# Kernel optimization log

Hardware: AMD Instinct MI355X
Metric: run time of the kernel (lower is better)

The kernel has to match this reference:

```python
import jax, jax.numpy as jnp
import numpy as np

H = 256      # hidden_dim
MEL = 80     # num_mel
R = 5        # reduction_factor
BS = 128
T_ENC = 512
T_DEC = 1000


def _gru_step(x, h, wih, whh, bih, bhh):
    # PyTorch GRU cell: gates order (r, z, n)
    gi = x @ wih.T + bih            # [bs, 3H]
    gh = h @ whh.T + bhh
    ir, iz, inn = jnp.split(gi, 3, axis=-1)
    hr, hz, hn = jnp.split(gh, 3, axis=-1)
    r = jax.nn.sigmoid(ir + hr)
    z = jax.nn.sigmoid(iz + hz)
    n = jnp.tanh(inn + r * hn)
    return (1.0 - z) * n + z * h


def setup_inputs() -> dict:
    key = jax.random.key(0)
    ks = iter(jax.random.split(key, 40))
    s = 0.05
    def w(shape):
        return jax.random.normal(next(ks), shape, dtype=jnp.float32) * s
    inp = {
        "enc_vec": jax.random.normal(next(ks), (BS, T_ENC, H), dtype=jnp.float32),
        "decoder_input": jax.random.normal(next(ks), (BS, T_DEC, MEL), dtype=jnp.float32),
        # Pre_net
        "pre_w1": w((H, MEL)), "pre_b1": jnp.zeros((H,), jnp.float32),
        "pre_w2": w((H // 2, H)), "pre_b2": jnp.zeros((H // 2,), jnp.float32),
        # Bahdanau attention
        "w1": w((H, H)), "b1": jnp.zeros((H,), jnp.float32),
        "w2": w((H, H)), "b2": jnp.zeros((H,), jnp.float32),
        "v_w": w((1, H)), "v_b": jnp.zeros((1,), jnp.float32),
        # projection and output
        "proj_w": w((H, 2 * H)), "proj_b": jnp.zeros((H,), jnp.float32),
        "out_w": w((MEL * R, H)), "out_b": jnp.zeros((MEL * R,), jnp.float32),
        # Attention GRU (input H//2)
        "att_wih": w((3 * H, H // 2)), "att_whh": w((3 * H, H)),
        "att_bih": jnp.zeros((3 * H,), jnp.float32), "att_bhh": jnp.zeros((3 * H,), jnp.float32),
        # GRU1, GRU2 (input H)
        "g1_wih": w((3 * H, H)), "g1_whh": w((3 * H, H)),
        "g1_bih": jnp.zeros((3 * H,), jnp.float32), "g1_bhh": jnp.zeros((3 * H,), jnp.float32),
        "g2_wih": w((3 * H, H)), "g2_whh": w((3 * H, H)),
        "g2_bih": jnp.zeros((3 * H,), jnp.float32), "g2_bhh": jnp.zeros((3 * H,), jnp.float32),
    }
    return inp


def reference(enc_vec, decoder_input, pre_w1, pre_b1, pre_w2, pre_b2,
              w1, b1, w2, b2, v_w, v_b, proj_w, proj_b, out_w, out_b,
              att_wih, att_whh, att_bih, att_bhh,
              g1_wih, g1_whh, g1_bih, g1_bhh,
              g2_wih, g2_whh, g2_bih, g2_bhh):
    bs = enc_vec.shape[0]
    # Pre_net (dropout omitted -> deterministic eval behavior)
    pre = jax.nn.relu(decoder_input @ pre_w1.T + pre_b1)
    pre = jax.nn.relu(pre @ pre_w2.T + pre_b2)          # [bs, T_dec, H//2]
    steps = decoder_input.shape[1] // R                 # 200
    # teacher-forced inputs: step i uses pre[:, i*R, :]
    xs = jnp.transpose(pre[:, :steps * R:R, :], (1, 0, 2))   # [steps, bs, H//2]
    # hoist W1(enc_vec): constant across decoder steps
    w1enc = enc_vec @ w1.T + b1                         # [bs, T_enc, H]

    h0 = jnp.zeros((bs, H), jnp.float32)

    def step(carry, x):
        ha, h1, h2 = carry
        d = _gru_step(x, ha, att_wih, att_whh, att_bih, att_bhh)   # [bs, H]
        e = jnp.tanh(w1enc + (d @ w2.T + b2)[:, None, :])          # [bs, T_enc, H]
        scores = e @ v_w[0] + v_b[0]                               # [bs, T_enc]
        u = jax.nn.softmax(scores, axis=1)
        d_dot = jnp.einsum('bt,bth->bh', u, enc_vec)               # [bs, H]
        p = jnp.concatenate([d, d_dot], axis=-1) @ proj_w.T + proj_b  # [bs, H]
        o1 = _gru_step(p, h1, g1_wih, g1_whh, g1_bih, g1_bhh)
        in2 = o1 + p
        o2 = _gru_step(in2, h2, g2_wih, g2_whh, g2_bih, g2_bhh)
        out = (in2 + o2) @ out_w.T + out_b                         # [bs, R*MEL]
        return (d, o1, o2), out

    _, ys = jax.lax.scan(step, (h0, h0, h0), xs)        # [steps, bs, R*MEL]
    ys = jnp.transpose(ys, (1, 0, 2)).reshape(bs, steps * R, MEL)
    return ys
```

## Files before the change

kernel.cpp:

```cpp
#include <hip/hip_runtime.h>
#include <hip/hip_bf16.h>

typedef unsigned short u16;
typedef unsigned int   u32;

constexpr int H     = 256;
constexpr int HH    = 128;
constexpr int MELD  = 80;
constexpr int RF    = 5;
constexpr int BS    = 128;
constexpr int TENC  = 512;
constexpr int TDEC  = 1000;
constexpr int STEPS = 200;
constexpr int OD    = 400;
constexpr int M_ALL = STEPS * BS;

constexpr size_t GI_B   = 0;
constexpr size_t ENC16_B= GI_B;
constexpr size_t D16_B  = GI_B   + (size_t)M_ALL*768*4;
constexpr size_t IN2_B  = D16_B;
constexpr size_t W1ET_B = D16_B  + (size_t)M_ALL*512*2;
constexpr size_t P16_B  = W1ET_B;
constexpr size_t IN2H_B = W1ET_B + (size_t)M_ALL*256*2;
constexpr size_t P_B    = W1ET_B + (size_t)BS*H*TENC*2;
constexpr size_t U16_B  = P_B;
constexpr size_t XSH_B  = P_B    + (size_t)M_ALL*256*4;
constexpr size_t ST16_B = XSH_B  + (size_t)M_ALL*128*2;
constexpr size_t WPK_B  = ST16_B + (size_t)M_ALL*256*2;
constexpr size_t WH_B   = WPK_B  + 3*(size_t)393216;
constexpr size_t WH_AW  = 0;
constexpr size_t WH_W2  = WH_AW + 98304*2;
constexpr size_t WH_PJ  = WH_W2 + 65536*2;
constexpr size_t WH_G1  = WH_PJ + 131072*2;
constexpr size_t WH_G2  = WH_G1 + 196608*2;
constexpr size_t WH_OW  = WH_G2 + 196608*2;
constexpr size_t WH_W1  = WH_OW + 102400*2;
constexpr size_t WH_END = WH_W1 + 65536*2;
constexpr size_t NEED_FAST = WH_B + WH_END;

constexpr size_t FBW1E_B  = 65536;
constexpr size_t FBXST_B  = FBW1E_B + (size_t)BS*TENC*H*2;
constexpr size_t FBF32_B  = FBXST_B + (size_t)STEPS*HH*BS*2;
constexpr size_t FBDT_F   = 0;
constexpr size_t FBO1_F   = FBDT_F + 2*(size_t)H*BS;
constexpr size_t FBO2_F   = FBO1_F + 2*(size_t)H*BS;
constexpr size_t FBPT_F   = FBO2_F + 2*(size_t)H*BS;
constexpr size_t FBIN2_F  = FBPT_F + (size_t)H*BS;
constexpr size_t FBST_F   = FBIN2_F + (size_t)H*BS;
constexpr size_t FB_NEED_B = FBF32_B + (FBST_F + 2*(size_t)H*BS) * 4;

__device__ __forceinline__ float bf2f(u16 v) {
  union { u32 x; float f; } c; c.x = ((u32)v) << 16; return c.f;
}
__device__ __forceinline__ float bfu_lo(u32 u) { union { u32 x; float f; } c; c.x = u << 16;        return c.f; }
__device__ __forceinline__ float bfu_hi(u32 u) { union { u32 x; float f; } c; c.x = u & 0xffff0000u; return c.f; }
__device__ __forceinline__ u16 f2bf(float f) {
  union { float f; u32 u; } c; c.f = f;
  u32 u = c.u;
  u32 r = (u + 0x7fffu + ((u >> 16) & 1u)) >> 16;
  return (u16)r;
}
__device__ __forceinline__ u16 f2h(float f) {
  union { _Float16 h; u16 u; } c; c.h = (_Float16)f; return c.u;
}
__device__ __forceinline__ float fexp(float x) {
  return __builtin_amdgcn_exp2f(1.4426950408889634f * x);
}
__device__ __forceinline__ float sigm_f(float x) {
  return __builtin_amdgcn_rcpf(1.0f + __builtin_amdgcn_exp2f(-1.4426950408889634f * x));
}
__device__ __forceinline__ float tanh_f(float x) {
  x = fminf(fmaxf(x, -15.f), 15.f);
  float e = __builtin_amdgcn_exp2f(2.8853900817779268f * x);
  return (e - 1.0f) * __builtin_amdgcn_rcpf(e + 1.0f);
}

typedef _Float16 hlf2 __attribute__((ext_vector_type(2)));
typedef _Float16 f16x8 __attribute__((ext_vector_type(8)));
typedef float f32x4 __attribute__((ext_vector_type(4)));

__global__ __launch_bounds__(256) void k_zero(float* __restrict__ out, int n) {
  int i = blockIdx.x * 256 + threadIdx.x;
  if (i < n) out[i] = 0.f;
}


__global__ __launch_bounds__(256) void k_prenet_f(
    const float* __restrict__ dec, const float* __restrict__ w1, const float* __restrict__ b1,
    const float* __restrict__ w2, const float* __restrict__ b2, u16* __restrict__ xsh)
{
  const int s = blockIdx.x, tid = threadIdx.x;
  __shared__ float X0[32][80];
  __shared__ float P1t[32][256];
  for (int bt = 0; bt < 4; ++bt) {
    const int b0 = bt * 32;
    __syncthreads();
    for (int i = tid; i < 32 * 80; i += 256) {
      int bb = i / 80, m = i - bb * 80;
      X0[bb][m] = dec[((size_t)(b0 + bb) * TDEC + (size_t)s * RF) * MELD + m];
    }
    __syncthreads();
    {
      const int h = tid;
      float acc[32];
      const float bias = b1[h];
      #pragma unroll
      for (int r = 0; r < 32; ++r) acc[r] = bias;
      const float* wr = w1 + (size_t)h * MELD;
      for (int m = 0; m < 80; m += 4) {
        float4 wv = *(const float4*)(wr + m);
        #pragma unroll
        for (int r = 0; r < 32; ++r) {
          float4 x = *(const float4*)&X0[r][m];
          acc[r] += x.x * wv.x + x.y * wv.y + x.z * wv.z + x.w * wv.w;
        }
      }
      #pragma unroll
      for (int r = 0; r < 32; ++r) P1t[r][h] = fmaxf(acc[r], 0.f);
    }
    __syncthreads();
    {
      const int k = tid & 127, bh = tid >> 7;
      float acc[16];
      const float bias = b2[k];
      #pragma unroll
      for (int r = 0; r < 16; ++r) acc[r] = bias;
      const float* wr = w2 + (size_t)k * H;
      for (int h = 0; h < H; h += 4) {
        float4 wv = *(const float4*)(wr + h);
        #pragma unroll
        for (int r = 0; r < 16; ++r) {
          float4 x = *(const float4*)&P1t[bh * 16 + r][h];
          acc[r] += x.x * wv.x + x.y * wv.y + x.z * wv.z + x.w * wv.w;
        }
      }
      #pragma unroll
      for (int r = 0; r < 16; ++r)
        xsh[((size_t)s * BS + b0 + bh * 16 + r) * HH + k] = f2h(fmaxf(acc[r], 0.f));
    }
  }
}

__global__ __launch_bounds__(256) void k_packall(
    const float* __restrict__ enc, u16* __restrict__ enc16,
    const float* __restrict__ awhh, const float* __restrict__ g1whh,
    const float* __restrict__ g2whh, u32* __restrict__ wpk,
    const float* __restrict__ awih, u16* __restrict__ awih16,
    const float* __restrict__ w2w,  u16* __restrict__ w2w16,
    const float* __restrict__ pjw,  u16* __restrict__ pjw16,
    const float* __restrict__ g1wih, u16* __restrict__ g1w16,
    const float* __restrict__ g2wih, u16* __restrict__ g2w16,
    const float* __restrict__ ow,   u16* __restrict__ ow16,
    const float* __restrict__ w1w,  u16* __restrict__ w1w16)
{
  int i = blockIdx.x * 256 + threadIdx.x;
  if (i < 16777216) { enc16[i] = f2h(enc[i]); return; }
  i -= 16777216;
  if (i < 294912) {
    int which = i / 98304, idx = i - which * 98304;
    const float* w = which == 0 ? awhh : (which == 1 ? g1whh : g2whh);
    int q  = idx & 3;
    int l  = (idx >> 2) & 63;
    int kt = (idx >> 8) & 7;
    int nt = idx >> 11;
    int col = nt * 16 + (l & 15);
    int k   = kt * 32 + (l >> 4) * 8 + 2 * q;
    union { _Float16 f[2]; u32 u; } c;
    c.f[0] = (_Float16)w[(size_t)col * 256 + k];
    c.f[1] = (_Float16)w[(size_t)col * 256 + k + 1];
    wpk[which * 98304 + idx] = c.u;
    return;
  }
  i -= 294912;
  if (i < 98304)  { awih16[i] = f2h(awih[i]); return; }  i -= 98304;
  if (i < 65536)  { w2w16[i]  = f2h(w2w[i]);  return; }  i -= 65536;
  if (i < 131072) { pjw16[i]  = f2h(pjw[i]);  return; }  i -= 131072;
  if (i < 196608) { g1w16[i]  = f2h(g1wih[i]); return; } i -= 196608;
  if (i < 196608) { g2w16[i]  = f2h(g2wih[i]); return; } i -= 196608;
  if (i < 102400) { ow16[i]   = f2h(ow[i]);   return; }  i -= 102400;
  if (i < 65536)  { w1w16[i]  = f2h(w1w[i]);  return; }
}
constexpr int PACKALL_N = 16777216 + 294912 + 856064;

__global__ __launch_bounds__(256) void k_hgemm(
    const u16* __restrict__ A, int lda,
    const u16* __restrict__ W, int K,
    const float* __restrict__ bias,
    float* __restrict__ C, u16* __restrict__ Ch, int ldc, int N,
    float* __restrict__ outmap, u16* __restrict__ CbfT)
{
  __shared__ _Float16 As[128 * 40];
  __shared__ _Float16 Ws[64 * 40];
  const int m0 = blockIdx.y * 128, n0 = blockIdx.x * 64;
  const int tid = threadIdx.x;
  const int wv = tid >> 6, lane = tid & 63;
  const int l15 = lane & 15, hi = lane >> 4;
  f32x4 acc[2][4];
  #pragma unroll
  for (int mi = 0; mi < 2; ++mi)
    #pragma unroll
    for (int ni = 0; ni < 4; ++ni) acc[mi][ni] = (f32x4){0.f, 0.f, 0.f, 0.f};

  const int ar = tid >> 1, ac = (tid & 1) * 16;
  const int wr = tid >> 2, wc = (tid & 3) * 8;
  for (int k0 = 0; k0 < K; k0 += 32) {
    __syncthreads();
    {
      const u16* src = A + (size_t)(m0 + ar) * lda + k0 + ac;
      uint4 v0 = *(const uint4*)(src);
      uint4 v1 = *(const uint4*)(src + 8);
      *(uint4*)&As[ar * 40 + ac] = v0;
      *(uint4*)&As[ar * 40 + ac + 8] = v1;
    }
    {
      uint4 v;
      if (n0 + wr < N) v = *(const uint4*)(W + (size_t)(n0 + wr) * K + k0 + wc);
      else { v.x = v.y = v.z = v.w = 0u; }
      *(uint4*)&Ws[wr * 40 + wc] = v;
    }
    __syncthreads();
    f16x8 af[2], bf[4];
    #pragma unroll
    for (int mi = 0; mi < 2; ++mi)
      af[mi] = *(const f16x8*)&As[(wv * 32 + mi * 16 + l15) * 40 + hi * 8];
    #pragma unroll
    for (int ni = 0; ni < 4; ++ni)
      bf[ni] = *(const f16x8*)&Ws[(ni * 16 + l15) * 40 + hi * 8];
    #pragma unroll
    for (int mi = 0; mi < 2; ++mi)
      #pragma unroll
      for (int ni = 0; ni < 4; ++ni)
        acc[mi][ni] = __builtin_amdgcn_mfma_f32_16x16x32_f16(af[mi], bf[ni], acc[mi][ni], 0, 0, 0);
  }
  const int gm = m0 + wv * 32;
  #pragma unroll
  for (int ni = 0; ni < 4; ++ni) {
    const int col = n0 + ni * 16 + l15;
    if (col < N) {
      const float bv = bias[col];
      #pragma unroll
      for (int mi = 0; mi < 2; ++mi) {
        #pragma unroll
        for (int r = 0; r < 4; ++r) {
          const int row = gm + mi * 16 + hi * 4 + r;
          float v = acc[mi][ni][r] + bv;
          if (outmap) {
            int s = row >> 7, b = row & 127;
            int fr = s * RF + col / MELD, mel = col - (col / MELD) * MELD;
            outmap[((size_t)b * TDEC + fr) * MELD + mel] = v;
          } else if (CbfT) {
            float a = fminf(fmaxf(2.8853900817779268f * v, -15.f), 15.f);
            CbfT[(((size_t)(row >> 9) * 256 + col) << 9) + (row & 511)] =
                f2bf(__builtin_amdgcn_exp2f(a));
          } else {
            if (C)  C[(size_t)row * ldc + col] = v;
            if (Ch) Ch[(size_t)row * ldc + col] = f2h(v);
          }
        }
      }
    }
  }
}

__global__ __launch_bounds__(256) void k_ddgemm(
    const u16* __restrict__ U, const float* __restrict__ enc,
    u16* __restrict__ D16)
{
  __shared__ _Float16 As[128 * 40];
  __shared__ _Float16 Ws[64 * 40];
  const int b = blockIdx.z;
  const int m0 = blockIdx.y * 128, n0 = blockIdx.x * 64;
  const int tid = threadIdx.x;
  const int wv = tid >> 6, lane = tid & 63;
  const int l15 = lane & 15, hi = lane >> 4;
  f32x4 acc[2][4];
  #pragma unroll
  for (int mi = 0; mi < 2; ++mi)
    #pragma unroll
    for (int ni = 0; ni < 4; ++ni) acc[mi][ni] = (f32x4){0.f, 0.f, 0.f, 0.f};

  const u16* A = U + (size_t)b * STEPS * TENC;
  const float* E = enc + (size_t)b * TENC * H;
  const int ar = tid >> 1, ac = (tid & 1) * 16;
  for (int k0 = 0; k0 < TENC; k0 += 32) {
    __syncthreads();
    {
      const u16* src = A + (size_t)(m0 + ar) * TENC + k0 + ac;
      uint4 v0 = *(const uint4*)(src);
      uint4 v1 = *(const uint4*)(src + 8);
      *(uint4*)&As[ar * 40 + ac] = v0;
      *(uint4*)&As[ar * 40 + ac + 8] = v1;
    }
    {
      #pragma unroll
      for (int it = 0; it < 2; ++it) {
        int flat = tid + it * 256;
        int kk = flat >> 4, hc4 = (flat & 15) * 4;
        float4 v = *(const float4*)(E + (size_t)(k0 + kk) * H + n0 + hc4);
        Ws[(hc4 + 0) * 40 + kk] = (_Float16)v.x;
        Ws[(hc4 + 1) * 40 + kk] = (_Float16)v.y;
        Ws[(hc4 + 2) * 40 + kk] = (_Float16)v.z;
        Ws[(hc4 + 3) * 40 + kk] = (_Float16)v.w;
      }
    }
    __syncthreads();
    f16x8 af[2], bf[4];
    #pragma unroll
    for (int mi = 0; mi < 2; ++mi)
      af[mi] = *(const f16x8*)&As[(wv * 32 + mi * 16 + l15) * 40 + hi * 8];
    #pragma unroll
    for (int ni = 0; ni < 4; ++ni)
      bf[ni] = *(const f16x8*)&Ws[(ni * 16 + l15) * 40 + hi * 8];
    #pragma unroll
    for (int mi = 0; mi < 2; ++mi)
      #pragma unroll
      for (int ni = 0; ni < 4; ++ni)
        acc[mi][ni] = __builtin_amdgcn_mfma_f32_16x16x32_f16(af[mi], bf[ni], acc[mi][ni], 0, 0, 0);
  }
  const int gm = m0 + wv * 32;
  #pragma unroll
  for (int ni = 0; ni < 4; ++ni) {
    const int col = n0 + ni * 16 + l15;
    #pragma unroll
    for (int mi = 0; mi < 2; ++mi) {
      #pragma unroll
      for (int r = 0; r < 4; ++r) {
        const int row = gm + mi * 16 + hi * 4 + r;
        if (row < STEPS)
          D16[((size_t)(row * BS + b)) * 512 + 256 + col] = f2h(acc[mi][ni][r]);
      }
    }
  }
}

__global__ __launch_bounds__(512) void k_chain(
    const float* __restrict__ gi,
    const uint4* __restrict__ wpkB,
    const float* __restrict__ bhh,
    const float* __restrict__ addsrc,
    int astride,
    float* __restrict__ outp, int ostride,
    u16* __restrict__ outph, int ostrideh)
{
  const int b = blockIdx.x, tid = threadIdx.x;
  const int wv = tid >> 6, lane = tid & 63;
  const int l15 = lane & 15, hi = lane >> 4;
  __shared__ __align__(16) _Float16 hf[256];
  __shared__ float gsh[768];
  f16x8 bfrag[6][8];
  #pragma unroll
  for (int nti = 0; nti < 6; ++nti)
    #pragma unroll
    for (int kt = 0; kt < 8; ++kt)
      bfrag[nti][kt] = *(const f16x8*)&wpkB[(((size_t)(wv * 6 + nti) * 8 + kt) * 64 + lane)];
  if (tid < 256) hf[tid] = (_Float16)0.f;
  const int j = tid;
  float br = 0.f, bz = 0.f, bn = 0.f, hreg = 0.f;
  float gr = 0.f, gz = 0.f, gn = 0.f, av = 0.f;
  if (tid < 256) {
    br = bhh[j]; bz = bhh[256 + j]; bn = bhh[512 + j];
    const float* gim = gi + (size_t)b * 768;
    gr = gim[j]; gz = gim[256 + j]; gn = gim[512 + j];
    if (addsrc) av = addsrc[(size_t)b * astride + j];
  }
  __syncthreads();
  for (int s = 0; s < STEPS; ++s) {
    f32x4 acc[6];
    #pragma unroll
    for (int nti = 0; nti < 6; ++nti) acc[nti] = (f32x4){0.f, 0.f, 0.f, 0.f};
    #pragma unroll
    for (int kt = 0; kt < 8; ++kt) {
      f16x8 af = *(const f16x8*)&hf[kt * 32 + hi * 8];
      #pragma unroll
      for (int nti = 0; nti < 6; ++nti)
        acc[nti] = __builtin_amdgcn_mfma_f32_16x16x32_f16(af, bfrag[nti][kt], acc[nti], 0, 0, 0);
    }
    float gr_n = 0.f, gz_n = 0.f, gn_n = 0.f, av_n = 0.f;
    if (tid < 256 && s + 1 < STEPS) {
      const size_t mn = (size_t)(s + 1) * BS + b;
      const float* gim = gi + mn * 768;
      gr_n = gim[j]; gz_n = gim[256 + j]; gn_n = gim[512 + j];
      if (addsrc) av_n = addsrc[mn * astride + j];
    }
    if (hi == 0) {
      #pragma unroll
      for (int nti = 0; nti < 6; ++nti)
        gsh[(wv * 6 + nti) * 16 + l15] = acc[nti][0];
    }
    __syncthreads();
    if (tid < 256) {
      const size_t m = (size_t)s * BS + b;
      float ar = gsh[j], az = gsh[256 + j], an = gsh[512 + j];
      float r = sigm_f(gr + ar + br);
      float z = sigm_f(gz + az + bz);
      float n = tanh_f(gn + r * (an + bn));
      float hn_ = (1.f - z) * n + z * hreg;
      hreg = hn_;
      hf[j] = (_Float16)hn_;
      float ov = hn_ + av;
      if (outp)  outp[m * ostride + j] = ov;
      if (outph) outph[m * ostrideh + j] = f2h(ov);
    }
    __syncthreads();
    gr = gr_n; gz = gz_n; gn = gn_n; av = av_n;
  }
}

constexpr int ATT_ST = 10;
__global__ __launch_bounds__(256) void k_att(
    const u16* __restrict__ w1eT, const float* __restrict__ Q,
    const float* __restrict__ vw_, u16* __restrict__ U16)
{
  const int b = blockIdx.x, s0 = blockIdx.y * ATT_ST, tid = threadIdx.x;
  __shared__ float qt[ATT_ST][260];
  __shared__ float vws[256];
  __shared__ float redw[ATT_ST][4];
  vws[tid] = -2.0f * vw_[tid];
  #pragma unroll
  for (int si = 0; si < ATT_ST; ++si) {
    float q = 2.8853900817779268f * Q[((size_t)(s0 + si) * BS + b) * H + tid];
    qt[si][tid] = __builtin_amdgcn_exp2f(fminf(fmaxf(q, -15.f), 15.f));
  }
  __syncthreads();

  float sc0[ATT_ST], sc1[ATT_ST];
  #pragma unroll
  for (int si = 0; si < ATT_ST; ++si) { sc0[si] = 0.f; sc1[si] = 0.f; }
  const u32* wrow = (const u32*)w1eT + (size_t)b * H * (TENC / 2);
  for (int h = 0; h < H; h += 4) {
    u32 wa = wrow[(size_t)(h + 0) * 256 + tid];
    u32 wb = wrow[(size_t)(h + 1) * 256 + tid];
    u32 wc = wrow[(size_t)(h + 2) * 256 + tid];
    u32 wd = wrow[(size_t)(h + 3) * 256 + tid];
    float Ea0 = bfu_lo(wa), Ea1 = bfu_hi(wa);
    float Eb0 = bfu_lo(wb), Eb1 = bfu_hi(wb);
    float Ec0 = bfu_lo(wc), Ec1 = bfu_hi(wc);
    float Ed0 = bfu_lo(wd), Ed1 = bfu_hi(wd);
    float4 vv = *(const float4*)&vws[h];
    #pragma unroll
    for (int si = 0; si < ATT_ST; ++si) {
      float4 Eq = *(const float4*)&qt[si][h];
      {
        float F1 = __builtin_fmaf(Ea0, Eq.x, 1.f);
        float F2 = __builtin_fmaf(Eb0, Eq.y, 1.f);
        float F3 = __builtin_fmaf(Ec0, Eq.z, 1.f);
        float F4 = __builtin_fmaf(Ed0, Eq.w, 1.f);
        float P12 = F1 * F2, P34 = F3 * F4;
        float u12 = __builtin_fmaf(vv.y, F1, vv.x * F2);
        float u34 = __builtin_fmaf(vv.w, F3, vv.z * F4);
        float num = __builtin_fmaf(P12, u34, P34 * u12);
        sc0[si] = __builtin_fmaf(num, __builtin_amdgcn_rcpf(P12 * P34), sc0[si]);
      }
      {
        float F1 = __builtin_fmaf(Ea1, Eq.x, 1.f);
        float F2 = __builtin_fmaf(Eb1, Eq.y, 1.f);
        float F3 = __builtin_fmaf(Ec1, Eq.z, 1.f);
        float F4 = __builtin_fmaf(Ed1, Eq.w, 1.f);
        float P12 = F1 * F2, P34 = F3 * F4;
        float u12 = __builtin_fmaf(vv.y, F1, vv.x * F2);
        float u34 = __builtin_fmaf(vv.w, F3, vv.z * F4);
        float num = __builtin_fmaf(P12, u34, P34 * u12);
        sc1[si] = __builtin_fmaf(num, __builtin_amdgcn_rcpf(P12 * P34), sc1[si]);
      }
    }
  }
  const int lane = tid & 63, wvi = tid >> 6;
  #pragma unroll
  for (int si = 0; si < ATT_ST; ++si) {
    float mw = fmaxf(sc0[si], sc1[si]);
    for (int off = 1; off < 64; off <<= 1) mw = fmaxf(mw, __shfl_xor(mw, off));
    if (lane == 0) redw[si][wvi] = mw;
  }
  __syncthreads();
  #pragma unroll
  for (int si = 0; si < ATT_ST; ++si) {
    float mx = fmaxf(fmaxf(redw[si][0], redw[si][1]), fmaxf(redw[si][2], redw[si][3]));
    sc0[si] = fexp(sc0[si] - mx);
    sc1[si] = fexp(sc1[si] - mx);
  }
  __syncthreads();
  #pragma unroll
  for (int si = 0; si < ATT_ST; ++si) {
    float sm = sc0[si] + sc1[si];
    for (int off = 1; off < 64; off <<= 1) sm += __shfl_xor(sm, off);
    if (lane == 0) redw[si][wvi] = sm;
  }
  __syncthreads();
  #pragma unroll
  for (int si = 0; si < ATT_ST; ++si) {
    float tot = redw[si][0] + redw[si][1] + redw[si][2] + redw[si][3];
    float li = __builtin_amdgcn_rcpf(tot);
    u32 pk = (u32)f2h(sc0[si] * li) | ((u32)f2h(sc1[si] * li) << 16);
    *(u32*)&U16[((size_t)b * STEPS + s0 + si) * TENC + 2 * tid] = pk;
  }
}

__global__ __launch_bounds__(256) void fbk_zeroinit(float* __restrict__ fst) {
  int i = blockIdx.x * 256 + threadIdx.x;
  if (i < H * BS)              fst[FBDT_F + i] = 0.f;
  else if (i < 2 * H * BS)     fst[FBO1_F + (i - H * BS)] = 0.f;
  else if (i < 3 * H * BS)     fst[FBO2_F + (i - 2 * H * BS)] = 0.f;
}

__global__ __launch_bounds__(256) void fbk_prenet(
    const float* __restrict__ dec, const float* __restrict__ w1, const float* __restrict__ b1,
    const float* __restrict__ w2, const float* __restrict__ b2, u16* __restrict__ xsT)
{
  const int s = blockIdx.x, tid = threadIdx.x;
  __shared__ float X0[32][80];
  __shared__ float P1t[32][256];
  for (int bt = 0; bt < 4; ++bt) {
    const int b0 = bt * 32;
    __syncthreads();
    for (int i = tid; i < 32 * 80; i += 256) {
      int bb = i / 80, m = i - bb * 80;
      X0[bb][m] = dec[((size_t)(b0 + bb) * TDEC + (size_t)s * RF) * MELD + m];
    }
    __syncthreads();
    {
      const int h = tid;
      float acc[32];
      const float bias = b1[h];
      #pragma unroll
      for (int r = 0; r < 32; ++r) acc[r] = bias;
      const float* wr = w1 + (size_t)h * MELD;
      for (int m = 0; m < 80; m += 4) {
        float4 wv = *(const float4*)(wr + m);
        #pragma unroll
        for (int r = 0; r < 32; ++r) {
          float4 x = *(const float4*)&X0[r][m];
          acc[r] += x.x * wv.x + x.y * wv.y + x.z * wv.z + x.w * wv.w;
        }
      }
      #pragma unroll
      for (int r = 0; r < 32; ++r) P1t[r][h] = fmaxf(acc[r], 0.f);
    }
    __syncthreads();
    {
      const int k = tid & 127, bh = tid >> 7;
      float acc[16];
      const float bias = b2[k];
      #pragma unroll
      for (int r = 0; r < 16; ++r) acc[r] = bias;
      const float* wr = w2 + (size_t)k * H;
      for (int h = 0; h < H; h += 4) {
        float4 wv = *(const float4*)(wr + h);
        #pragma unroll
        for (int r = 0; r < 16; ++r) {
          float4 x = *(const float4*)&P1t[bh * 16 + r][h];
          acc[r] += x.x * wv.x + x.y * wv.y + x.z * wv.z + x.w * wv.w;
        }
      }
      #pragma unroll
      for (int r = 0; r < 16; ++r)
        xsT[((size_t)s * HH + k) * BS + b0 + bh * 16 + r] = f2bf(fmaxf(acc[r], 0.f));
    }
  }
}

__global__ __launch_bounds__(256) void fbk_w1enc(
    const float* __restrict__ enc, const float* __restrict__ w1, const float* __restrict__ b1,
    u16* __restrict__ w1e)
{
  const int row0 = blockIdx.x * 32;
  const int tid = threadIdx.x;
  __shared__ float A[32 * 256];
  for (int i = tid * 4; i < 32 * 256; i += 256 * 4) {
    float4 v = *(const float4*)(enc + (size_t)row0 * H + i);
    A[i] = v.x; A[i + 1] = v.y; A[i + 2] = v.z; A[i + 3] = v.w;
  }
  __syncthreads();
  const int h = tid;
  float acc[32];
  const float bias = b1[h];
  #pragma unroll
  for (int r = 0; r < 32; ++r) acc[r] = bias;
  const float* wr = w1 + (size_t)h * H;
  for (int k = 0; k < H; k += 4) {
    float4 wv = *(const float4*)(wr + k);
    #pragma unroll
    for (int r = 0; r < 32; ++r) {
      float4 a = *(const float4*)&A[r * 256 + k];
      acc[r] += a.x * wv.x + a.y * wv.y + a.z * wv.z + a.w * wv.w;
    }
  }
  #pragma unroll
  for (int r = 0; r < 32; ++r) w1e[((size_t)row0 + r) * H + h] = f2bf(acc[r]);
}

__device__ __forceinline__ void fb_gru_body(
    float (*w6)[260], float (*pA)[128], float (*pB)[128], int j, int tid,
    const float* __restrict__ gi_src, const float* __restrict__ h_src,
    const float* __restrict__ wih, const float* __restrict__ whh,
    const float* __restrict__ bih, const float* __restrict__ bhh,
    float* __restrict__ h_out, float* __restrict__ sum_out)
{
  for (int i = tid; i < 3 * H; i += 256) {
    int gg = i >> 8, k = i & 255;
    w6[gg][k]     = wih[((size_t)gg * H + j) * H + k];
    w6[3 + gg][k] = whh[((size_t)gg * H + j) * H + k];
  }
  __syncthreads();
  const int b = tid & 127, kh = tid >> 7;
  float pr = 0, pz = 0, pn = 0, hr = 0, hz = 0, hn = 0;
  for (int k = kh * 128; k < kh * 128 + 128; k += 4) {
    float4 wia = *(const float4*)&w6[0][k];
    float4 wib = *(const float4*)&w6[1][k];
    float4 wic = *(const float4*)&w6[2][k];
    float4 wha = *(const float4*)&w6[3][k];
    float4 whb = *(const float4*)&w6[4][k];
    float4 whc = *(const float4*)&w6[5][k];
    float x0 = gi_src[(size_t)(k + 0) * BS + b], x1 = gi_src[(size_t)(k + 1) * BS + b];
    float x2 = gi_src[(size_t)(k + 2) * BS + b], x3 = gi_src[(size_t)(k + 3) * BS + b];
    float h0 = h_src[(size_t)(k + 0) * BS + b],  h1 = h_src[(size_t)(k + 1) * BS + b];
    float h2 = h_src[(size_t)(k + 2) * BS + b],  h3 = h_src[(size_t)(k + 3) * BS + b];
    pr += x0 * wia.x + x1 * wia.y + x2 * wia.z + x3 * wia.w;
    pz += x0 * wib.x + x1 * wib.y + x2 * wib.z + x3 * wib.w;
    pn += x0 * wic.x + x1 * wic.y + x2 * wic.z + x3 * wic.w;
    hr += h0 * wha.x + h1 * wha.y + h2 * wha.z + h3 * wha.w;
    hz += h0 * whb.x + h1 * whb.y + h2 * whb.z + h3 * whb.w;
    hn += h0 * whc.x + h1 * whc.y + h2 * whc.z + h3 * whc.w;
  }
  if (kh) {
    pA[0][b] = pr; pA[1][b] = pz; pA[2][b] = pn;
    pB[0][b] = hr; pB[1][b] = hz; pB[2][b] = hn;
  }
  __syncthreads();
  if (!kh) {
    float gir = pr + pA[0][b] + bih[j];
    float giz = pz + pA[1][b] + bih[H + j];
    float gin = pn + pA[2][b] + bih[2 * H + j];
    float ghr = hr + pB[0][b] + bhh[j];
    float ghz = hz + pB[1][b] + bhh[H + j];
    float ghn = hn + pB[2][b] + bhh[2 * H + j];
    float r = sigm_f(gir + ghr);
    float z = sigm_f(giz + ghz);
    float n = tanh_f(gin + r * ghn);
    float hp = h_src[(size_t)j * BS + b];
    float o = (1.f - z) * n + z * hp;
    h_out[(size_t)j * BS + b] = o;
    if (sum_out) sum_out[(size_t)j * BS + b] = o + gi_src[(size_t)j * BS + b];
  }
}

__global__ __launch_bounds__(256) void fbk_attgru(
    const u16* __restrict__ xstu, float* __restrict__ fst,
    const float* __restrict__ awih, const float* __restrict__ awhh,
    const float* __restrict__ abih, const float* __restrict__ abhh, int s)
{
  const int j = blockIdx.x, tid = threadIdx.x;
  __shared__ float w6[6][260];
  __shared__ float pA[3][128];
  __shared__ float pB[3][128];
  const float* dprev = fst + FBDT_F + (size_t)(s & 1) * H * BS;
  float*       dcur  = fst + FBDT_F + (size_t)((s + 1) & 1) * H * BS;
  for (int i = tid; i < 3 * HH; i += 256) {
    int gg = i >> 7, k = i & (HH - 1);
    w6[gg][k] = awih[((size_t)gg * H + j) * HH + k];
  }
  for (int i = tid; i < 3 * H; i += 256) {
    int gg = i >> 8, k = i & (H - 1);
    w6[3 + gg][k] = awhh[((size_t)gg * H + j) * H + k];
  }
  __syncthreads();
  const u16* xcol = xstu + (size_t)s * HH * BS;
  const int b = tid & 127, kh = tid >> 7;
  float pr = 0, pz = 0, pn = 0, hr = 0, hz = 0, hn = 0;
  for (int k = kh * 64; k < kh * 64 + 64; k += 4) {
    float4 wa = *(const float4*)&w6[0][k];
    float4 wb = *(const float4*)&w6[1][k];
    float4 wc = *(const float4*)&w6[2][k];
    float x0 = bf2f(xcol[(size_t)(k + 0) * BS + b]), x1 = bf2f(xcol[(size_t)(k + 1) * BS + b]);
    float x2 = bf2f(xcol[(size_t)(k + 2) * BS + b]), x3 = bf2f(xcol[(size_t)(k + 3) * BS + b]);
    pr += x0 * wa.x + x1 * wa.y + x2 * wa.z + x3 * wa.w;
    pz += x0 * wb.x + x1 * wb.y + x2 * wb.z + x3 * wb.w;
    pn += x0 * wc.x + x1 * wc.y + x2 * wc.z + x3 * wc.w;
  }
  for (int k = kh * 128; k < kh * 128 + 128; k += 4) {
    float4 wa = *(const float4*)&w6[3][k];
    float4 wb = *(const float4*)&w6[4][k];
    float4 wc = *(const float4*)&w6[5][k];
    float h0 = dprev[(size_t)(k + 0) * BS + b], h1 = dprev[(size_t)(k + 1) * BS + b];
    float h2 = dprev[(size_t)(k + 2) * BS + b], h3 = dprev[(size_t)(k + 3) * BS + b];
    hr += h0 * wa.x + h1 * wa.y + h2 * wa.z + h3 * wa.w;
    hz += h0 * wb.x + h1 * wb.y + h2 * wb.z + h3 * wb.w;
    hn += h0 * wc.x + h1 * wc.y + h2 * wc.z + h3 * wc.w;
  }
  if (kh) {
    pA[0][b] = pr; pA[1][b] = pz; pA[2][b] = pn;
    pB[0][b] = hr; pB[1][b] = hz; pB[2][b] = hn;
  }
  __syncthreads();
  if (!kh) {
    float gir = pr + pA[0][b] + abih[j];
    float giz = pz + pA[1][b] + abih[H + j];
    float gin = pn + pA[2][b] + abih[2 * H + j];
    float ghr = hr + pB[0][b] + abhh[j];
    float ghz = hz + pB[1][b] + abhh[H + j];
    float ghn = hn + pB[2][b] + abhh[2 * H + j];
    float r = sigm_f(gir + ghr);
    float z = sigm_f(giz + ghz);
    float n = tanh_f(gin + r * ghn);
    float hp = dprev[(size_t)j * BS + b];
    dcur[(size_t)j * BS + b] = (1.f - z) * n + z * hp;
  }
}

__global__ __launch_bounds__(256) void fbk_attn(
    const float* __restrict__ enc, const u16* __restrict__ w1eu,
    const float* __restrict__ w2w, const float* __restrict__ b2w,
    const float* __restrict__ vww, const float* __restrict__ vbw,
    const float* __restrict__ pjw, const float* __restrict__ pjb,
    float* __restrict__ fst, int s)
{
  const int b3 = blockIdx.x, tid = threadIdx.x;
  __shared__ float dsh[256], qs[256], ddh[256], vwsh[256], ev[512], red[256];
  const float* dcur = fst + FBDT_F + (size_t)((s + 1) & 1) * H * BS;
  float* pT = fst + FBPT_F;
  dsh[tid]  = dcur[(size_t)tid * BS + b3];
  vwsh[tid] = vww[tid];
  __syncthreads();
  {
    const int jj = tid;
    const float* wr = w2w + (size_t)jj * H;
    float acc = b2w[jj];
    for (int k = 0; k < H; k += 8) {
      float4 wA = *(const float4*)(wr + k);
      float4 wB = *(const float4*)(wr + k + 4);
      float4 dA = *(const float4*)&dsh[k];
      float4 dB = *(const float4*)&dsh[k + 4];
      acc += dA.x * wA.x + dA.y * wA.y + dA.z * wA.z + dA.w * wA.w
           + dB.x * wB.x + dB.y * wB.y + dB.z * wB.z + dB.w * wB.w;
    }
    qs[jj] = acc;
  }
  __syncthreads();
  const float vbf = vbw[0];
  const u16* wr0 = w1eu + ((size_t)b3 * TENC + tid) * H;
  const u16* wr1 = wr0 + (size_t)256 * H;
  float sc0 = vbf, sc1 = vbf;
  for (int h = 0; h < H; h += 8) {
    uint4 ua = *(const uint4*)(wr0 + h);
    uint4 uc = *(const uint4*)(wr1 + h);
    float4 qA = *(const float4*)&qs[h];
    float4 qB = *(const float4*)&qs[h + 4];
    float4 vA = *(const float4*)&vwsh[h];
    float4 vB = *(const float4*)&vwsh[h + 4];
    sc0 += vA.x * tanh_f(bfu_lo(ua.x) + qA.x) + vA.y * tanh_f(bfu_hi(ua.x) + qA.y)
         + vA.z * tanh_f(bfu_lo(ua.y) + qA.z) + vA.w * tanh_f(bfu_hi(ua.y) + qA.w)
         + vB.x * tanh_f(bfu_lo(ua.z) + qB.x) + vB.y * tanh_f(bfu_hi(ua.z) + qB.y)
         + vB.z * tanh_f(bfu_lo(ua.w) + qB.z) + vB.w * tanh_f(bfu_hi(ua.w) + qB.w);
    sc1 += vA.x * tanh_f(bfu_lo(uc.x) + qA.x) + vA.y * tanh_f(bfu_hi(uc.x) + qA.y)
         + vA.z * tanh_f(bfu_lo(uc.y) + qA.z) + vA.w * tanh_f(bfu_hi(uc.y) + qA.w)
         + vB.x * tanh_f(bfu_lo(uc.z) + qB.x) + vB.y * tanh_f(bfu_hi(uc.z) + qB.y)
         + vB.z * tanh_f(bfu_lo(uc.w) + qB.z) + vB.w * tanh_f(bfu_hi(uc.w) + qB.w);
  }
  red[tid] = fmaxf(sc0, sc1);
  __syncthreads();
  for (int off = 128; off > 0; off >>= 1) {
    if (tid < off) red[tid] = fmaxf(red[tid], red[tid + off]);
    __syncthreads();
  }
  float mx = red[0];
  __syncthreads();
  float e0 = fexp(sc0 - mx), e1 = fexp(sc1 - mx);
  ev[tid] = e0; ev[256 + tid] = e1;
  red[tid] = e0 + e1;
  __syncthreads();
  for (int off = 128; off > 0; off >>= 1) {
    if (tid < off) red[tid] += red[tid + off];
    __syncthreads();
  }
  float linv = __builtin_amdgcn_rcpf(red[0]);
  __syncthreads();
  {
    float vacc = 0.f;
    const float* ep = enc + (size_t)b3 * TENC * H + tid;
    for (int tt = 0; tt < TENC; tt += 4) {
      float4 e4 = *(const float4*)&ev[tt];
      vacc += e4.x * ep[(size_t)(tt + 0) * H] + e4.y * ep[(size_t)(tt + 1) * H]
            + e4.z * ep[(size_t)(tt + 2) * H] + e4.w * ep[(size_t)(tt + 3) * H];
    }
    ddh[tid] = vacc * linv;
  }
  __syncthreads();
  {
    const int jj = tid;
    const float* wr = pjw + (size_t)jj * (2 * H);
    float acc = pjb[jj];
    for (int k = 0; k < H; k += 8) {
      float4 wA = *(const float4*)(wr + k);
      float4 wB = *(const float4*)(wr + k + 4);
      float4 dA = *(const float4*)&dsh[k];
      float4 dB = *(const float4*)&dsh[k + 4];
      acc += dA.x * wA.x + dA.y * wA.y + dA.z * wA.z + dA.w * wA.w
           + dB.x * wB.x + dB.y * wB.y + dB.z * wB.z + dB.w * wB.w;
    }
    for (int k = 0; k < H; k += 8) {
      float4 wA = *(const float4*)(wr + H + k);
      float4 wB = *(const float4*)(wr + H + k + 4);
      float4 dA = *(const float4*)&ddh[k];
      float4 dB = *(const float4*)&ddh[k + 4];
      acc += dA.x * wA.x + dA.y * wA.y + dA.z * wA.z + dA.w * wA.w
           + dB.x * wB.x + dB.y * wB.y + dB.z * wB.z + dB.w * wB.w;
    }
    pT[(size_t)jj * BS + b3] = acc;
  }
}

__global__ __launch_bounds__(256) void fbk_gru1(
    float* __restrict__ fst,
    const float* __restrict__ wih, const float* __restrict__ whh,
    const float* __restrict__ bih, const float* __restrict__ bhh, int s)
{
  __shared__ float w6[6][260];
  __shared__ float pA[3][128];
  __shared__ float pB[3][128];
  const float* pT     = fst + FBPT_F;
  const float* o1prev = fst + FBO1_F + (size_t)(s & 1) * H * BS;
  float*       o1cur  = fst + FBO1_F + (size_t)((s + 1) & 1) * H * BS;
  float*       in2T   = fst + FBIN2_F;
  fb_gru_body(w6, pA, pB, blockIdx.x, threadIdx.x, pT, o1prev, wih, whh, bih, bhh, o1cur, in2T);
}

__device__ __forceinline__ void fb_out_body(
    float (*pA)[128], int bb, int tid, int s,
    const float* __restrict__ sT, const float* __restrict__ ow,
    const float* __restrict__ ob, float* __restrict__ out)
{
  const int b = tid & 127, kh = tid >> 7;
  for (int r = bb; r < OD; r += 128) {
    const float* wr = ow + (size_t)r * H + kh * 128;
    float acc = 0.f;
    for (int kk = 0; kk < 128; kk += 4) {
      float4 wv = *(const float4*)(wr + kk);
      const float* sp = sT + (size_t)(kh * 128 + kk) * BS + b;
      acc += sp[0] * wv.x + sp[BS] * wv.y + sp[2 * BS] * wv.z + sp[3 * BS] * wv.w;
    }
    __syncthreads();
    if (kh) pA[0][b] = acc;
    __syncthreads();
    if (!kh) {
      float y = acc + pA[0][b] + ob[r];
      int frame = s * RF + r / MELD;
      int m = r - (r / MELD) * MELD;
      out[((size_t)b * TDEC + frame) * MELD + m] = y;
    }
  }
}

__global__ __launch_bounds__(256) void fbk_gru2out(
    float* __restrict__ fst,
    const float* __restrict__ wih, const float* __restrict__ whh,
    const float* __restrict__ bih, const float* __restrict__ bhh,
    const float* __restrict__ ow, const float* __restrict__ ob,
    float* __restrict__ out, int s)
{
  const int bid = blockIdx.x, tid = threadIdx.x;
  __shared__ float w6[6][260];
  __shared__ float pA[3][128];
  __shared__ float pB[3][128];
  if (bid < 256) {
    const float* in2T   = fst + FBIN2_F;
    const float* o2prev = fst + FBO2_F + (size_t)(s & 1) * H * BS;
    float*       o2cur  = fst + FBO2_F + (size_t)((s + 1) & 1) * H * BS;
    float*       stp    = fst + FBST_F + (size_t)(s & 1) * H * BS;
    fb_gru_body(w6, pA, pB, bid, tid, in2T, o2prev, wih, whh, bih, bhh, o2cur, stp);
  } else if (s > 0) {
    const float* sT = fst + FBST_F + (size_t)((s - 1) & 1) * H * BS;
    fb_out_body(pA, bid - 256, tid, s - 1, sT, ow, ob, out);
  }
}

__global__ __launch_bounds__(256) void fbk_outlast(
    const float* __restrict__ fst, const float* __restrict__ ow,
    const float* __restrict__ ob, float* __restrict__ out)
{
  __shared__ float pA[3][128];
  const float* sT = fst + FBST_F + (size_t)((STEPS - 1) & 1) * H * BS;
  fb_out_body(pA, blockIdx.x, threadIdx.x, STEPS - 1, sT, ow, ob, out);
}

extern "C" void kernel_launch(void* const* d_in, const int* in_sizes, int n_in,
                              void* d_out, int out_size, void* d_ws, size_t ws_size,
                              hipStream_t stream) {
  const float* enc   = (const float*)d_in[0];
  const float* dec   = (const float*)d_in[1];
  const float* pw1   = (const float*)d_in[2];
  const float* pb1   = (const float*)d_in[3];
  const float* pw2   = (const float*)d_in[4];
  const float* pb2   = (const float*)d_in[5];
  const float* w1w   = (const float*)d_in[6];
  const float* b1w   = (const float*)d_in[7];
  const float* w2w   = (const float*)d_in[8];
  const float* b2w   = (const float*)d_in[9];
  const float* vww   = (const float*)d_in[10];
  const float* vbw   = (const float*)d_in[11];
  const float* pjw   = (const float*)d_in[12];
  const float* pjb   = (const float*)d_in[13];
  const float* ow    = (const float*)d_in[14];
  const float* ob    = (const float*)d_in[15];
  const float* awih  = (const float*)d_in[16];
  const float* awhh  = (const float*)d_in[17];
  const float* abih  = (const float*)d_in[18];
  const float* abhh  = (const float*)d_in[19];
  const float* g1wih = (const float*)d_in[20];
  const float* g1whh = (const float*)d_in[21];
  const float* g1bih = (const float*)d_in[22];
  const float* g1bhh = (const float*)d_in[23];
  const float* g2wih = (const float*)d_in[24];
  const float* g2whh = (const float*)d_in[25];
  const float* g2bih = (const float*)d_in[26];
  const float* g2bhh = (const float*)d_in[27];
  float* out = (float*)d_out;
  char* wsb = (char*)d_ws;

  if (ws_size >= NEED_FAST) {
    float* GI   = (float*)(wsb + GI_B);
    u16*   ENC16= (u16*)(wsb + ENC16_B);
    u16*   D16  = (u16*)(wsb + D16_B);
    float* IN2  = (float*)(wsb + IN2_B);
    u16*   w1eT = (u16*)(wsb + W1ET_B);
    u16*   P16  = (u16*)(wsb + P16_B);
    u16*   IN2H = (u16*)(wsb + IN2H_B);
    float* P    = (float*)(wsb + P_B);
    u16*   U16  = (u16*)(wsb + U16_B);
    u16*   XSH  = (u16*)(wsb + XSH_B);
    u16*   ST16 = (u16*)(wsb + ST16_B);
    u32*   wpkA = (u32*)(wsb + WPK_B);
    u32*   wpk1 = wpkA + 98304;
    u32*   wpk2 = wpk1 + 98304;
    u16*   awih16 = (u16*)(wsb + WH_B + WH_AW);
    u16*   w2w16  = (u16*)(wsb + WH_B + WH_W2);
    u16*   pjw16  = (u16*)(wsb + WH_B + WH_PJ);
    u16*   g1w16  = (u16*)(wsb + WH_B + WH_G1);
    u16*   g2w16  = (u16*)(wsb + WH_B + WH_G2);
    u16*   ow16   = (u16*)(wsb + WH_B + WH_OW);
    u16*   w1w16  = (u16*)(wsb + WH_B + WH_W1);

    k_packall<<<PACKALL_N / 256, 256, 0, stream>>>(
        enc, ENC16, awhh, g1whh, g2whh, wpkA,
        awih, awih16, w2w, w2w16, pjw, pjw16, g1wih, g1w16,
        g2wih, g2w16, ow, ow16, w1w, w1w16);
    k_hgemm<<<dim3(4, (BS * TENC) / 128), 256, 0, stream>>>(
        ENC16, H, w1w16, H, b1w, nullptr, nullptr, 0, 256, nullptr, w1eT);
    k_prenet_f<<<STEPS, 256, 0, stream>>>(dec, pw1, pb1, pw2, pb2, XSH);
    k_hgemm<<<dim3(12, M_ALL / 128), 256, 0, stream>>>(XSH, HH, awih16, HH, abih, GI, nullptr, 768, 768, nullptr, nullptr);
    k_chain<<<BS, 512, 0, stream>>>(GI, (const uint4*)wpkA, abhh, nullptr, 0, nullptr, 0, D16, 512);
    k_hgemm<<<dim3(4, M_ALL / 128), 256, 0, stream>>>(D16, 512, w2w16, H, b2w, GI, nullptr, 256, 256, nullptr, nullptr);
    k_att<<<dim3(BS, STEPS / ATT_ST), 256, 0, stream>>>(w1eT, GI, vww, U16);
    k_ddgemm<<<dim3(4, 2, BS), 256, 0, stream>>>(U16, enc, D16);
    k_hgemm<<<dim3(4, M_ALL / 128), 256, 0, stream>>>(D16, 512, pjw16, 2 * H, pjb, P, P16, 256, 256, nullptr, nullptr);
    k_hgemm<<<dim3(12, M_ALL / 128), 256, 0, stream>>>(P16, H, g1w16, H, g1bih, GI, nullptr, 768, 768, nullptr, nullptr);
    k_chain<<<BS, 512, 0, stream>>>(GI, (const uint4*)wpk1, g1bhh, P, 256, IN2, 256, IN2H, 256);
    k_hgemm<<<dim3(12, M_ALL / 128), 256, 0, stream>>>(IN2H, H, g2w16, H, g2bih, GI, nullptr, 768, 768, nullptr, nullptr);
    k_chain<<<BS, 512, 0, stream>>>(GI, (const uint4*)wpk2, g2bhh, IN2, 256, nullptr, 0, ST16, 256);
    k_hgemm<<<dim3(7, M_ALL / 128), 256, 0, stream>>>(ST16, H, ow16, H, ob, nullptr, nullptr, 0, OD, out, nullptr);
    return;
  }

  if (ws_size < FB_NEED_B) {
    k_zero<<<(out_size + 255) / 256, 256, 0, stream>>>(out, out_size);
    return;
  }

  u16*  w1eu = (u16*)(wsb + FBW1E_B);
  u16*  xstu = (u16*)(wsb + FBXST_B);
  float* fst = (float*)(wsb + FBF32_B);

  fbk_zeroinit<<<384, 256, 0, stream>>>(fst);
  fbk_prenet<<<STEPS, 256, 0, stream>>>(dec, pw1, pb1, pw2, pb2, xstu);
  fbk_w1enc<<<(BS * TENC) / 32, 256, 0, stream>>>(enc, w1w, b1w, w1eu);
  for (int s = 0; s < STEPS; ++s) {
    fbk_attgru<<<256, 256, 0, stream>>>(xstu, fst, awih, awhh, abih, abhh, s);
    fbk_attn<<<BS, 256, 0, stream>>>(enc, w1eu, w2w, b2w, vww, vbw, pjw, pjb, fst, s);
    fbk_gru1<<<256, 256, 0, stream>>>(fst, g1wih, g1whh, g1bih, g1bhh, s);
    fbk_gru2out<<<384, 256, 0, stream>>>(fst, g2wih, g2whh, g2bih, g2bhh, ow, ob, out, s);
  }
  fbk_outlast<<<BS, 256, 0, stream>>>(fst, ow, ob, out);
}
```

Before: 1.568 ms.

## Permute GRU recurrent weight columns so each wave computes its own gates

Repacks the recurrent weight matrix so that each wave's six MFMA column tiles hold the r, z and n gate columns for the same 32 hidden units. The gate nonlinearity can then run straight from accumulator registers, with no shared-memory gate buffer. The hidden state is double-buffered in LDS, so only one barrier per step is needed instead of two. Only the 16 lanes with hi==0 do the elementwise work, each handling two units, which lowers parallelism in that phase.

```diff
diff --git a/kernel.cpp b/kernel.cpp
--- a/kernel.cpp
+++ b/kernel.cpp
@@ -163,7 +163,8 @@
     int l  = (idx >> 2) & 63;
     int kt = (idx >> 8) & 7;
     int nt = idx >> 11;
-    int col = nt * 16 + (l & 15);
+    int wv = nt / 6, nti = nt - wv * 6;
+    int col = (nti >> 1) * 256 + wv * 32 + (nti & 1) * 16 + (l & 15);
     int k   = kt * 32 + (l >> 4) * 8 + 2 * q;
     union { _Float16 f[2]; u32 u; } c;
     c.f[0] = (_Float16)w[(size_t)col * 256 + k];
@@ -345,64 +346,87 @@
   const int b = blockIdx.x, tid = threadIdx.x;
   const int wv = tid >> 6, lane = tid & 63;
   const int l15 = lane & 15, hi = lane >> 4;
-  __shared__ __align__(16) _Float16 hf[256];
-  __shared__ float gsh[768];
+  __shared__ __align__(16) _Float16 hf[2][256];
   f16x8 bfrag[6][8];
   #pragma unroll
   for (int nti = 0; nti < 6; ++nti)
     #pragma unroll
     for (int kt = 0; kt < 8; ++kt)
       bfrag[nti][kt] = *(const f16x8*)&wpkB[(((size_t)(wv * 6 + nti) * 8 + kt) * 64 + lane)];
-  if (tid < 256) hf[tid] = (_Float16)0.f;
-  const int j = tid;
-  float br = 0.f, bz = 0.f, bn = 0.f, hreg = 0.f;
-  float gr = 0.f, gz = 0.f, gn = 0.f, av = 0.f;
-  if (tid < 256) {
-    br = bhh[j]; bz = bhh[256 + j]; bn = bhh[512 + j];
-    const float* gim = gi + (size_t)b * 768;
-    gr = gim[j]; gz = gim[256 + j]; gn = gim[512 + j];
-    if (addsrc) av = addsrc[(size_t)b * astride + j];
-  }
-  __syncthreads();
+  if (tid < 256) hf[0][tid] = (_Float16)0.f;
+  const bool gl = (hi == 0);
+  const int j0 = wv * 32 + l15, j1 = j0 + 16;
+  float br0 = 0.f, bz0 = 0.f, bn0 = 0.f, br1 = 0.f, bz1 = 0.f, bn1 = 0.f;
+  float h0reg = 0.f, h1reg = 0.f;
+  float gr0 = 0.f, gz0 = 0.f, gn0 = 0.f, av0 = 0.f;
+  float gr1 = 0.f, gz1 = 0.f, gn1 = 0.f, av1 = 0.f;
+  if (gl) {
+    br0 = bhh[j0]; bz0 = bhh[256 + j0]; bn0 = bhh[512 + j0];
+    br1 = bhh[j1]; bz1 = bhh[256 + j1]; bn1 = bhh[512 + j1];
+    const float* g0 = gi + (size_t)b * 768;
+    gr0 = g0[j0]; gz0 = g0[256 + j0]; gn0 = g0[512 + j0];
+    gr1 = g0[j1]; gz1 = g0[256 + j1]; gn1 = g0[512 + j1];
+    if (addsrc) {
+      av0 = addsrc[(size_t)b * astride + j0];
+      av1 = addsrc[(size_t)b * astride + j1];
+    }
+  }
+  __syncthreads();
+  int p = 0;
   for (int s = 0; s < STEPS; ++s) {
+    float grA0 = 0.f, gzA0 = 0.f, gnA0 = 0.f, avA0 = 0.f;
+    float grA1 = 0.f, gzA1 = 0.f, gnA1 = 0.f, avA1 = 0.f;
+    if (gl && s + 1 < STEPS) {
+      const size_t mn = (size_t)(s + 1) * BS + b;
+      const float* gp = gi + mn * 768;
+      grA0 = gp[j0]; gzA0 = gp[256 + j0]; gnA0 = gp[512 + j0];
+      grA1 = gp[j1]; gzA1 = gp[256 + j1]; gnA1 = gp[512 + j1];
+      if (addsrc) {
+        avA0 = addsrc[mn * astride + j0];
+        avA1 = addsrc[mn * astride + j1];
+      }
+    }
     f32x4 acc[6];
     #pragma unroll
     for (int nti = 0; nti < 6; ++nti) acc[nti] = (f32x4){0.f, 0.f, 0.f, 0.f};
     #pragma unroll
     for (int kt = 0; kt < 8; ++kt) {
-      f16x8 af = *(const f16x8*)&hf[kt * 32 + hi * 8];
+      f16x8 af = *(const f16x8*)&hf[p][kt * 32 + hi * 8];
       #pragma unroll
       for (int nti = 0; nti < 6; ++nti)
         acc[nti] = __builtin_amdgcn_mfma_f32_16x16x32_f16(af, bfrag[nti][kt], acc[nti], 0, 0, 0);
     }
-    float gr_n = 0.f, gz_n = 0.f, gn_n = 0.f, av_n = 0.f;
-    if (tid < 256 && s + 1 < STEPS) {
-      const size_t mn = (size_t)(s + 1) * BS + b;
-      const float* gim = gi + mn * 768;
-      gr_n = gim[j]; gz_n = gim[256 + j]; gn_n = gim[512 + j];
-      if (addsrc) av_n = addsrc[mn * astride + j];
-    }
-    if (hi == 0) {
-      #pragma unroll
-      for (int nti = 0; nti < 6; ++nti)
-        gsh[(wv * 6 + nti) * 16 + l15] = acc[nti][0];
-    }
-    __syncthreads();
-    if (tid < 256) {
+    if (gl) {
       const size_t m = (size_t)s * BS + b;
-      float ar = gsh[j], az = gsh[256 + j], an = gsh[512 + j];
-      float r = sigm_f(gr + ar + br);
-      float z = sigm_f(gz + az + bz);
-      float n = tanh_f(gn + r * (an + bn));
-      float hn_ = (1.f - z) * n + z * hreg;
-      hreg = hn_;
-      hf[j] = (_Float16)hn_;
-      float ov = hn_ + av;
-      if (outp)  outp[m * ostride + j] = ov;
-      if (outph) outph[m * ostrideh + j] = f2h(ov);
-    }
-    __syncthreads();
-    gr = gr_n; gz = gz_n; gn = gn_n; av = av_n;
+      float ar0 = acc[0][0], az0 = acc[2][0], an0 = acc[4][0];
+      float ar1 = acc[1][0], az1 = acc[3][0], an1 = acc[5][0];
+      {
+        float r = sigm_f(gr0 + ar0 + br0);
+        float z = sigm_f(gz0 + az0 + bz0);
+        float n = tanh_f(gn0 + r * (an0 + bn0));
+        float hn_ = (1.f - z) * n + z * h0reg;
+        h0reg = hn_;
+        hf[p ^ 1][j0] = (_Float16)hn_;
+        float ov = hn_ + av0;
+        if (outp)  outp[m * ostride + j0] = ov;
+        if (outph) outph[m * ostrideh + j0] = f2h(ov);
+      }
+      {
+        float r = sigm_f(gr1 + ar1 + br1);
+        float z = sigm_f(gz1 + az1 + bz1);
+        float n = tanh_f(gn1 + r * (an1 + bn1));
+        float hn_ = (1.f - z) * n + z * h1reg;
+        h1reg = hn_;
+        hf[p ^ 1][j1] = (_Float16)hn_;
+        float ov = hn_ + av1;
+        if (outp)  outp[m * ostride + j1] = ov;
+        if (outph) outph[m * ostrideh + j1] = f2h(ov);
+      }
+    }
+    __syncthreads();
+    p ^= 1;
+    gr0 = grA0; gz0 = gzA0; gn0 = gnA0; av0 = avA0;
+    gr1 = grA1; gz1 = gzA1; gn1 = gnA1; av1 = avA1;
   }
 }
 
```

Result: slower. 2.061 ms (+31.5%).
